# Kernel optimization log

Hardware: AMD Instinct MI355X
Metric: run time of the kernel (lower is better)

The kernel has to match this reference:

```python
import jax, jax.numpy as jnp
import numpy as np

N = 1024
D_IN = 512
D = 128
E = 8192


def setup_inputs() -> dict:
    key = jax.random.key(0)
    ks = jax.random.split(key, 7)
    return {
        "inputs": jax.random.normal(ks[0], (N, D_IN), dtype=jnp.float32),
        "adj": jax.random.uniform(ks[1], (N, N), dtype=jnp.float32),
        "weight": jax.random.normal(ks[2], (D_IN, D), dtype=jnp.float32) * 0.05,
        "weight_two": jax.random.normal(ks[3], (2 * D, D), dtype=jnp.float32) * 0.05,
        "weight_three": jax.random.normal(ks[4], (2 * D, 1), dtype=jnp.float32) * 0.05,
        "train_edges": jax.random.randint(ks[5], (E, 2), 0, N, dtype=jnp.int64 if jax.config.jax_enable_x64 else jnp.int32),
        "train_false_edges": jax.random.randint(ks[6], (E, 2), 0, N, dtype=jnp.int64 if jax.config.jax_enable_x64 else jnp.int32),
    }


def reference(inputs, adj, weight, weight_two, weight_three, train_edges, train_false_edges):
    # encoder: x = X W ; z = A x   (single GCN-style layer, no bias)
    x = inputs @ weight          # (N, D)
    z = adj @ x                  # (N, D)
    n, d = z.shape

    # all-pairs features: pair (i, j) -> [z_i ; z_j]  (torch repeat/reshape semantics)
    z1 = jnp.broadcast_to(z[:, None, :], (n, n, d))   # z1[i,j] = z[i]
    z2 = jnp.broadcast_to(z[None, :, :], (n, n, d))   # z2[i,j] = z[j]

    z_pair = jax.nn.relu(jnp.concatenate([z1, z2], axis=-1))   # (N, N, 2D)
    z_pair = jnp.einsum('ijk,kl->ijl', z_pair, weight_two)     # (N, N, D)
    z_em = z1 * z2                                             # (N, N, D)

    score = jnp.einsum('ijk,kl->ijl', jnp.concatenate([z_pair, z_em], axis=-1), weight_three)
    return jax.nn.sigmoid(score[..., 0])  # (N, N)
```

## Files before the change

### kernel.cpp

```cpp
#include <hip/hip_runtime.h>
#include <math.h>

#define NN 1024
#define DIN 512
#define DD 128

static constexpr long X_OFF = 0;
static constexpr long Z_OFF = X_OFF + (long)NN * DD;
static constexpr long U_OFF = Z_OFF + (long)NN * DD;
static constexpr long A_OFF = U_OFF + 256;
static constexpr long B_OFF = A_OFF + NN;

__global__ __launch_bounds__(1024, 4) void k1_x_u(
    const float* __restrict__ inputs, const float* __restrict__ W,
    const float* __restrict__ W2, const float* __restrict__ w3,
    float* __restrict__ x, float* __restrict__ u) {
  __shared__ float arow[8 * DIN];
  const int t = threadIdx.x;
  const int blk = blockIdx.x;

  ((float4*)arow)[t] = ((const float4*)(inputs + (long)blk * 8 * DIN))[t];
  __syncthreads();

  const int c = t & 127;
  const int rh = t >> 7;
  const float* wp = W + c;
  const float* ap = arow + rh * DIN;
  float acc = 0.f;
#pragma unroll 16
  for (int k = 0; k < DIN; ++k) acc += ap[k] * wp[(long)k * DD];
  x[(long)(blk * 8 + rh) * DD + c] = acc;

  if (blk < 8 && t < 256) {
    const int row = blk * 32 + (t >> 3);
    const int l8 = t & 7;
    float s = 0.f;
#pragma unroll
    for (int i = 0; i < 16; ++i) {
      const int l = l8 + 8 * i;
      s += W2[(long)row * DD + l] * w3[l];
    }
#pragma unroll
    for (int off = 4; off > 0; off >>= 1) s += __shfl_down(s, off, 8);
    if (l8 == 0) u[row] = s;
  }
}

__global__ __launch_bounds__(1024, 4) void k2_z_ab(
    const float* __restrict__ adj, const float* __restrict__ x,
    const float* __restrict__ u, float* __restrict__ z,
    float* __restrict__ a, float* __restrict__ b) {
  __shared__ float arow[8 * NN];
  __shared__ float red[16][2];
  const int t = threadIdx.x;
  const int blk = blockIdx.x;

  const float4* src = (const float4*)(adj + (long)blk * 8 * NN);
#pragma unroll
  for (int s = 0; s < 2; ++s) ((float4*)arow)[s * 1024 + t] = src[s * 1024 + t];
  __syncthreads();

  const int c = t & 127;
  const int rh = t >> 7;
  const float* xp = x + c;
  const float* ap = arow + rh * NN;
  float acc = 0.f;
#pragma unroll 16
  for (int k = 0; k < NN; ++k) acc += ap[k] * xp[(long)k * DD];
  const int row = blk * 8 + rh;
  z[(long)row * DD + c] = acc;

  const float r = acc > 0.f ? acc : 0.f;
  float pa = r * u[c];
  float pb = r * u[DD + c];
#pragma unroll
  for (int off = 32; off > 0; off >>= 1) {
    pa += __shfl_down(pa, off);
    pb += __shfl_down(pb, off);
  }
  const int w = t >> 6;
  if ((t & 63) == 0) { red[w][0] = pa; red[w][1] = pb; }
  __syncthreads();
  if (t < 8) {
    a[blk * 8 + t] = red[2 * t][0] + red[2 * t + 1][0];
    b[blk * 8 + t] = red[2 * t][1] + red[2 * t + 1][1];
  }
}

__global__ __launch_bounds__(256) void decode_tile(
    const float* __restrict__ z, const float* __restrict__ w3,
    const float* __restrict__ a, const float* __restrict__ b,
    float* __restrict__ out) {
  __shared__ float zl[64 * DD];
  __shared__ float zwl[64 * DD];
  const int t = threadIdx.x;
  const int i0 = blockIdx.y * 64;
  const int j0 = blockIdx.x * 64;

#pragma unroll
  for (int s = 0; s < 8; ++s) {
    const int q = s * 256 + t;
    const int r = q >> 5;
    const int k4 = (q & 31) << 2;
    const int sw = r * DD + (k4 ^ ((r & 7) << 2));
    *(float4*)&zl[sw] = *(const float4*)&z[(long)(i0 + r) * DD + k4];
    float4 w = *(const float4*)&z[(long)(j0 + r) * DD + k4];
    const float4 c = *(const float4*)&w3[DD + k4];
    w.x *= c.x; w.y *= c.y; w.z *= c.z; w.w *= c.w;
    *(float4*)&zwl[sw] = w;
  }
  __syncthreads();

  const int tx = t & 15;
  const int ty = t >> 4;
  float acc[4][4] = {};
  for (int k4 = 0; k4 < DD; k4 += 4) {
    float4 ar[4], bc[4];
#pragma unroll
    for (int m = 0; m < 4; ++m) {
      const int R = ty + 16 * m;
      ar[m] = *(const float4*)&zl[R * DD + (k4 ^ ((R & 7) << 2))];
    }
#pragma unroll
    for (int m = 0; m < 4; ++m) {
      const int C = tx + 16 * m;
      bc[m] = *(const float4*)&zwl[C * DD + (k4 ^ ((C & 7) << 2))];
    }
#pragma unroll
    for (int mr = 0; mr < 4; ++mr)
#pragma unroll
      for (int mc = 0; mc < 4; ++mc)
        acc[mr][mc] += ar[mr].x * bc[mc].x + ar[mr].y * bc[mc].y +
                       ar[mr].z * bc[mc].z + ar[mr].w * bc[mc].w;
  }

#pragma unroll
  for (int mr = 0; mr < 4; ++mr) {
    const int i = i0 + ty + 16 * mr;
    const float ai = a[i];
#pragma unroll
    for (int mc = 0; mc < 4; ++mc) {
      const int j = j0 + tx + 16 * mc;
      const float s = ai + b[j] + acc[mr][mc];
      out[(long)i * NN + j] = 1.0f / (1.0f + __expf(-s));
    }
  }
}

extern "C" void kernel_launch(void* const* d_in, const int* in_sizes, int n_in,
                              void* d_out, int out_size, void* d_ws, size_t ws_size,
                              hipStream_t stream) {
  (void)in_sizes; (void)n_in; (void)out_size; (void)ws_size;
  const float* inputs = (const float*)d_in[0];
  const float* adj    = (const float*)d_in[1];
  const float* weight = (const float*)d_in[2];
  const float* W2     = (const float*)d_in[3];
  const float* w3     = (const float*)d_in[4];
  float* out = (float*)d_out;

  float* ws = (float*)d_ws;
  float* x = ws + X_OFF;
  float* z = ws + Z_OFF;
  float* u = ws + U_OFF;
  float* a = ws + A_OFF;
  float* b = ws + B_OFF;

  k1_x_u<<<128, 1024, 0, stream>>>(inputs, weight, W2, w3, x, u);
  k2_z_ab<<<128, 1024, 0, stream>>>(adj, x, u, z, a, b);
  decode_tile<<<dim3(16, 16), 256, 0, stream>>>(z, w3, a, b, out);
}
```

Before: 126.5 us.

## Split-K atomic adj@x, fold z zeroing into x GEMM, compute a/b in decode

```diff
diff --git a/kernel.cpp b/kernel.cpp
--- a/kernel.cpp
+++ b/kernel.cpp
@@ -8,28 +8,41 @@
 static constexpr long X_OFF = 0;
 static constexpr long Z_OFF = X_OFF + (long)NN * DD;
 static constexpr long U_OFF = Z_OFF + (long)NN * DD;
-static constexpr long A_OFF = U_OFF + 256;
-static constexpr long B_OFF = A_OFF + NN;
 
-__global__ __launch_bounds__(1024, 4) void k1_x_u(
+__global__ __launch_bounds__(512) void k1_x_zeroz_u(
     const float* __restrict__ inputs, const float* __restrict__ W,
     const float* __restrict__ W2, const float* __restrict__ w3,
-    float* __restrict__ x, float* __restrict__ u) {
-  __shared__ float arow[8 * DIN];
+    float* __restrict__ x, float* __restrict__ z, float* __restrict__ u) {
   const int t = threadIdx.x;
-  const int blk = blockIdx.x;
+  const int bx = blockIdx.x;
+  const int by = blockIdx.y;
+  const int blk = bx * 4 + by;
 
-  ((float4*)arow)[t] = ((const float4*)(inputs + (long)blk * 8 * DIN))[t];
-  __syncthreads();
+  if (t < 256) {
+    float4 zz; zz.x = 0.f; zz.y = 0.f; zz.z = 0.f; zz.w = 0.f;
+    ((float4*)z)[(long)blk * 256 + t] = zz;
+  }
 
-  const int c = t & 127;
-  const int rh = t >> 7;
-  const float* wp = W + c;
-  const float* ap = arow + rh * DIN;
-  float acc = 0.f;
-#pragma unroll 16
-  for (int k = 0; k < DIN; ++k) acc += ap[k] * wp[(long)k * DD];
-  x[(long)(blk * 8 + rh) * DD + c] = acc;
+  const int tx = t & 31;
+  const int ty = t >> 5;
+  const int c  = by * 32 + tx;
+  const int r0 = bx * 32 + ty;
+  const float* A0 = inputs + (long)r0 * DIN;
+  const float* A1 = inputs + (long)(r0 + 16) * DIN;
+  float acc0 = 0.f, acc1 = 0.f;
+#pragma unroll 4
+  for (int k = 0; k < DIN; k += 4) {
+    const float4 a0 = *(const float4*)&A0[k];
+    const float4 a1 = *(const float4*)&A1[k];
+    const float b0 = W[(long)k * DD + c];
+    const float b1 = W[(long)(k + 1) * DD + c];
+    const float b2 = W[(long)(k + 2) * DD + c];
+    const float b3 = W[(long)(k + 3) * DD + c];
+    acc0 += a0.x * b0 + a0.y * b1 + a0.z * b2 + a0.w * b3;
+    acc1 += a1.x * b0 + a1.y * b1 + a1.z * b2 + a1.w * b3;
+  }
+  x[(long)r0 * DD + c] = acc0;
+  x[(long)(r0 + 16) * DD + c] = acc1;
 
   if (blk < 8 && t < 256) {
     const int row = blk * 32 + (t >> 3);
@@ -46,53 +59,52 @@
   }
 }
 
-__global__ __launch_bounds__(1024, 4) void k2_z_ab(
+__global__ __launch_bounds__(256) void k2_z_atomic(
     const float* __restrict__ adj, const float* __restrict__ x,
-    const float* __restrict__ u, float* __restrict__ z,
-    float* __restrict__ a, float* __restrict__ b) {
-  __shared__ float arow[8 * NN];
-  __shared__ float red[16][2];
+    float* __restrict__ z) {
   const int t = threadIdx.x;
-  const int blk = blockIdx.x;
+  const int tx = t & 31;
+  const int ty = t >> 5;
+  const int row0 = blockIdx.x * 32;
+  const int k0 = blockIdx.y * 128;
 
-  const float4* src = (const float4*)(adj + (long)blk * 8 * NN);
+  float acc[4][4] = {};
+
+  for (int k = k0; k < k0 + 128; k += 4) {
+    float bv[4][4];
 #pragma unroll
-  for (int s = 0; s < 2; ++s) ((float4*)arow)[s * 1024 + t] = src[s * 1024 + t];
-  __syncthreads();
+    for (int kk = 0; kk < 4; ++kk) {
+      const float* Brow = &x[(long)(k + kk) * DD + tx];
+#pragma unroll
+      for (int mc = 0; mc < 4; ++mc) bv[kk][mc] = Brow[32 * mc];
+    }
+#pragma unroll
+    for (int mr = 0; mr < 4; ++mr) {
+      const int r = row0 + ty + 8 * mr;
+      const float4 av = *(const float4*)&adj[(long)r * NN + k];
+      const float ar[4] = {av.x, av.y, av.z, av.w};
+#pragma unroll
+      for (int kk = 0; kk < 4; ++kk)
+#pragma unroll
+        for (int mc = 0; mc < 4; ++mc) acc[mr][mc] += ar[kk] * bv[kk][mc];
+    }
+  }
 
-  const int c = t & 127;
-  const int rh = t >> 7;
-  const float* xp = x + c;
-  const float* ap = arow + rh * NN;
-  float acc = 0.f;
-#pragma unroll 16
-  for (int k = 0; k < NN; ++k) acc += ap[k] * xp[(long)k * DD];
-  const int row = blk * 8 + rh;
-  z[(long)row * DD + c] = acc;
-
-  const float r = acc > 0.f ? acc : 0.f;
-  float pa = r * u[c];
-  float pb = r * u[DD + c];
 #pragma unroll
-  for (int off = 32; off > 0; off >>= 1) {
-    pa += __shfl_down(pa, off);
-    pb += __shfl_down(pb, off);
-  }
-  const int w = t >> 6;
-  if ((t & 63) == 0) { red[w][0] = pa; red[w][1] = pb; }
-  __syncthreads();
-  if (t < 8) {
-    a[blk * 8 + t] = red[2 * t][0] + red[2 * t + 1][0];
-    b[blk * 8 + t] = red[2 * t][1] + red[2 * t + 1][1];
+  for (int mr = 0; mr < 4; ++mr) {
+    const int r = row0 + ty + 8 * mr;
+#pragma unroll
+    for (int mc = 0; mc < 4; ++mc)
+      atomicAdd(&z[(long)r * DD + tx + 32 * mc], acc[mr][mc]);
   }
 }
 
-__global__ __launch_bounds__(256) void decode_tile(
+__global__ __launch_bounds__(256) void k3_decode(
     const float* __restrict__ z, const float* __restrict__ w3,
-    const float* __restrict__ a, const float* __restrict__ b,
-    float* __restrict__ out) {
-  __shared__ float zl[64 * DD];
+    const float* __restrict__ u, float* __restrict__ out) {
   __shared__ float zwl[64 * DD];
+  __shared__ float a_loc[64];
+  __shared__ float b_loc[64];
   const int t = threadIdx.x;
   const int i0 = blockIdx.y * 64;
   const int j0 = blockIdx.x * 64;
@@ -102,12 +114,23 @@
     const int q = s * 256 + t;
     const int r = q >> 5;
     const int k4 = (q & 31) << 2;
-    const int sw = r * DD + (k4 ^ ((r & 7) << 2));
-    *(float4*)&zl[sw] = *(const float4*)&z[(long)(i0 + r) * DD + k4];
+    const float4 u0 = *(const float4*)&u[k4];
+    const float4 u1 = *(const float4*)&u[DD + k4];
+    const float4 v = *(const float4*)&z[(long)(i0 + r) * DD + k4];
+    float pa = fmaxf(v.x, 0.f) * u0.x + fmaxf(v.y, 0.f) * u0.y +
+               fmaxf(v.z, 0.f) * u0.z + fmaxf(v.w, 0.f) * u0.w;
     float4 w = *(const float4*)&z[(long)(j0 + r) * DD + k4];
-    const float4 c = *(const float4*)&w3[DD + k4];
-    w.x *= c.x; w.y *= c.y; w.z *= c.z; w.w *= c.w;
-    *(float4*)&zwl[sw] = w;
+    float pb = fmaxf(w.x, 0.f) * u1.x + fmaxf(w.y, 0.f) * u1.y +
+               fmaxf(w.z, 0.f) * u1.z + fmaxf(w.w, 0.f) * u1.w;
+    const float4 cc = *(const float4*)&w3[DD + k4];
+    w.x *= cc.x; w.y *= cc.y; w.z *= cc.z; w.w *= cc.w;
+    *(float4*)&zwl[r * DD + (k4 ^ ((r & 7) << 2))] = w;
+#pragma unroll
+    for (int off = 16; off > 0; off >>= 1) {
+      pa += __shfl_down(pa, off, 32);
+      pb += __shfl_down(pb, off, 32);
+    }
+    if ((t & 31) == 0) { a_loc[r] = pa; b_loc[r] = pb; }
   }
   __syncthreads();
 
@@ -117,10 +140,8 @@
   for (int k4 = 0; k4 < DD; k4 += 4) {
     float4 ar[4], bc[4];
 #pragma unroll
-    for (int m = 0; m < 4; ++m) {
-      const int R = ty + 16 * m;
-      ar[m] = *(const float4*)&zl[R * DD + (k4 ^ ((R & 7) << 2))];
-    }
+    for (int m = 0; m < 4; ++m)
+      ar[m] = *(const float4*)&z[(long)(i0 + ty + 16 * m) * DD + k4];
 #pragma unroll
     for (int m = 0; m < 4; ++m) {
       const int C = tx + 16 * m;
@@ -137,11 +158,11 @@
 #pragma unroll
   for (int mr = 0; mr < 4; ++mr) {
     const int i = i0 + ty + 16 * mr;
-    const float ai = a[i];
+    const float ai = a_loc[ty + 16 * mr];
 #pragma unroll
     for (int mc = 0; mc < 4; ++mc) {
       const int j = j0 + tx + 16 * mc;
-      const float s = ai + b[j] + acc[mr][mc];
+      const float s = ai + b_loc[tx + 16 * mc] + acc[mr][mc];
       out[(long)i * NN + j] = 1.0f / (1.0f + __expf(-s));
     }
   }
@@ -162,10 +183,8 @@
   float* x = ws + X_OFF;
   float* z = ws + Z_OFF;
   float* u = ws + U_OFF;
-  float* a = ws + A_OFF;
-  float* b = ws + B_OFF;
 
-  k1_x_u<<<128, 1024, 0, stream>>>(inputs, weight, W2, w3, x, u);
-  k2_z_ab<<<128, 1024, 0, stream>>>(adj, x, u, z, a, b);
-  decode_tile<<<dim3(16, 16), 256, 0, stream>>>(z, w3, a, b, out);
+  k1_x_zeroz_u<<<dim3(32, 4), 512, 0, stream>>>(inputs, weight, W2, w3, x, z, u);
+  k2_z_atomic<<<dim3(32, 8), 256, 0, stream>>>(adj, x, z);
+  k3_decode<<<dim3(16, 16), 256, 0, stream>>>(z, w3, u, out);
 }
```

Measured after the change: 126.8 us. About the same (+0.3%).
